# Performance work log

Measured on AMD Instinct MI355X. Metric: run time of the kernel, lower is better.

The kernel has to match this reference:

```python
import jax, jax.numpy as jnp
import numpy as np

T, B, D, H, OUT = 128, 256, 512, 768, 60


def setup_inputs() -> dict:
    key = jax.random.key(0)
    ks = jax.random.split(key, 8)
    def xavier(k, shape):
        fan_out, fan_in = shape
        limit = np.sqrt(6.0 / (fan_in + fan_out))
        return jax.random.uniform(k, shape, jnp.float32, -limit, limit)
    inp = {
        "input_sample": jax.random.normal(ks[0], (T, B, D), jnp.float32),
        # PyTorch LSTMCell params: weight_ih (4H, D), weight_hh (4H, H), biases (4H,)
        "W_ih": xavier(ks[1], (4 * H, D)),
        "W_hh": xavier(ks[2], (4 * H, H)),
        "b_ih": jax.random.uniform(ks[3], (4 * H,), jnp.float32, -1 / np.sqrt(H), 1 / np.sqrt(H)),
        "b_hh": jax.random.uniform(ks[4], (4 * H,), jnp.float32, -1 / np.sqrt(H), 1 / np.sqrt(H)),
        "W_fc": xavier(ks[5], (OUT, H)),
        "b_fc": jnp.zeros((OUT,), jnp.float32),
    }
    return inp


def _lstm_head(input_sample, W_ih, W_hh, b_ih, b_hh, W_fc, b_fc):
    B_ = input_sample.shape[1]
    H_ = W_hh.shape[1]
    # Precompute input projections for all time steps in one GEMM: (T, B, 4H)
    x_proj = jnp.einsum("tbd,gd->tbg", input_sample, W_ih) + b_ih + b_hh

    def step(carry, xp_t):
        h, c = carry
        gates = xp_t + h @ W_hh.T  # (B, 4H)
        i, f, g, o = jnp.split(gates, 4, axis=-1)  # PyTorch gate order: i, f, g, o
        i = jax.nn.sigmoid(i)
        f = jax.nn.sigmoid(f)
        g = jnp.tanh(g)
        o = jax.nn.sigmoid(o)
        c_new = f * c + i * g
        h_new = o * jnp.tanh(c_new)
        return (h_new, c_new), None

    h0 = jnp.zeros((B_, H_), input_sample.dtype)
    c0 = jnp.zeros((B_, H_), input_sample.dtype)
    (h_T, _), _ = jax.lax.scan(step, (h0, c0), x_proj)
    return h_T @ W_fc.T + b_fc  # (B, OUT)


def reference(input_sample, W_ih, W_hh, b_ih, b_hh, W_fc, b_fc):
    return _lstm_head(input_sample, W_ih, W_hh, b_ih, b_hh, W_fc, b_fc)
```

## Files before the change

### kernel.cpp

```cpp
#include <hip/hip_runtime.h>
#include <stdint.h>

#define T_ 128
#define B_ 256
#define D_ 512
#define H_ 768
#define OUT_ 60

using bf16x8 = __attribute__((ext_vector_type(8))) __bf16;
using f32x4  = __attribute__((ext_vector_type(4))) float;
using u32x4  = __attribute__((ext_vector_type(4))) unsigned int;

#define OFF_XPK  ((size_t)0)
#define OFF_WIPK (OFF_XPK + (size_t)T_*B_*D_*2)
#define OFF_WHPK (OFF_WIPK + (size_t)4*H_*D_*2)
#define OFF_H    (OFF_WHPK + (size_t)4*H_*H_*2)
#define OFF_HT   (OFF_H + (size_t)2*B_*H_*2)
#define OFF_BAR  (OFF_HT + (size_t)B_*H_*4)
#define OFF_END  (OFF_BAR + 65536)

__device__ __forceinline__ unsigned short f2bf(float f) {
  union { float f; unsigned u; } v; v.f = f;
  unsigned r = (v.u + 0x7fffu + ((v.u >> 16) & 1u)) >> 16;
  return (unsigned short)r;
}
__device__ __forceinline__ float sigf(float x) {
  return __builtin_amdgcn_rcpf(1.0f + __expf(-x));
}
__device__ __forceinline__ float tanhf_(float x) {
  return 2.0f * __builtin_amdgcn_rcpf(1.0f + __expf(-2.0f * x)) - 1.0f;
}
__device__ __forceinline__ void gload16(const void* g, void* l) {
  __builtin_amdgcn_global_load_lds(
      (const __attribute__((address_space(1))) unsigned int*)g,
      (__attribute__((address_space(3))) unsigned int*)l, 16, 0, 0);
}
template<int OFF, bool SC1>
__device__ __forceinline__ u32x4 ld16(const void* p) {
  u32x4 r;
  if constexpr (SC1)
    asm volatile("global_load_dwordx4 %0, %1, off offset:%c2 sc0 sc1"
                 : "=v"(r) : "v"(p), "i"(OFF) : "memory");
  else
    asm volatile("global_load_dwordx4 %0, %1, off offset:%c2 sc0"
                 : "=v"(r) : "v"(p), "i"(OFF) : "memory");
  return r;
}
template<bool SC1>
__device__ __forceinline__ unsigned ld4w(const unsigned* p) {
  unsigned r;
  if constexpr (SC1)
    asm volatile("global_load_dword %0, %1, off sc0 sc1\n\ts_waitcnt vmcnt(0)"
                 : "=v"(r) : "v"(p) : "memory");
  else
    asm volatile("global_load_dword %0, %1, off sc0\n\ts_waitcnt vmcnt(0)"
                 : "=v"(r) : "v"(p) : "memory");
  return r;
}
template<bool SC1>
__device__ __forceinline__ void st2(ushort* p, unsigned v) {
  if constexpr (SC1)
    asm volatile("global_store_short %0, %1, off sc0 sc1" :: "v"(p), "v"(v) : "memory");
  else
    asm volatile("global_store_short %0, %1, off sc0" :: "v"(p), "v"(v) : "memory");
}
template<bool SC1>
__device__ __forceinline__ void st4(unsigned* p, unsigned v) {
  if constexpr (SC1)
    asm volatile("global_store_dword %0, %1, off sc0 sc1" :: "v"(p), "v"(v) : "memory");
  else
    asm volatile("global_store_dword %0, %1, off sc0" :: "v"(p), "v"(v) : "memory");
}

__global__ void prep_kernel(const float* __restrict__ x,
                            const float* __restrict__ wihf,
                            const float* __restrict__ whhf,
                            uint8_t* __restrict__ ws) {
  ushort* xpk = (ushort*)(ws + OFF_XPK);
  ushort* wipk = (ushort*)(ws + OFF_WIPK);
  ushort* whpk = (ushort*)(ws + OFF_WHPK);
  unsigned* bar = (unsigned*)(ws + OFF_BAR);
  const size_t tid = (size_t)blockIdx.x * blockDim.x + threadIdx.x;
  const size_t nth = (size_t)gridDim.x * blockDim.x;

  for (size_t c = tid; c < (size_t)T_*B_*D_/8; c += nth) {
    const unsigned row = (unsigned)(c >> 6);
    const unsigned j = (unsigned)c & 63u;
    const unsigned t = row >> 8, b = row & 255u;
    const float4 v0 = ((const float4*)x)[c*2];
    const float4 v1 = ((const float4*)x)[c*2+1];
    ushort4 o0, o1;
    o0.x=f2bf(v0.x); o0.y=f2bf(v0.y); o0.z=f2bf(v0.z); o0.w=f2bf(v0.w);
    o1.x=f2bf(v1.x); o1.y=f2bf(v1.y); o1.z=f2bf(v1.z); o1.w=f2bf(v1.w);
    const size_t dst = ((size_t)(((t*8u + (b>>5))*2u + ((b>>4)&1u))*16u + (j>>2))*64u
                        + (j&3u)*16u + (b&15u)) * 8u;
    *(ushort4*)(xpk + dst)     = o0;
    *(ushort4*)(xpk + dst + 4) = o1;
  }
  for (size_t c = tid; c < (size_t)196608; c += nth) {
    const unsigned L = (unsigned)c & 63u;
    const unsigned r1 = (unsigned)(c >> 6);
    const unsigned nt = r1 % 6u, r2 = r1 / 6u;
    const unsigned kf = r2 & 15u, s = r2 >> 4;
    const unsigned i = nt*16u + (L & 15u);
    const unsigned G = (i & 3u)*768u + s*24u + (i >> 2);
    const unsigned k0 = kf*32u + (L >> 4)*8u;
    const float4 v0 = *(const float4*)(wihf + (size_t)G*512u + k0);
    const float4 v1 = *(const float4*)(wihf + (size_t)G*512u + k0 + 4);
    ushort4 o0, o1;
    o0.x=f2bf(v0.x); o0.y=f2bf(v0.y); o0.z=f2bf(v0.z); o0.w=f2bf(v0.w);
    o1.x=f2bf(v1.x); o1.y=f2bf(v1.y); o1.z=f2bf(v1.z); o1.w=f2bf(v1.w);
    *(ushort4*)(wipk + c*8)     = o0;
    *(ushort4*)(wipk + c*8 + 4) = o1;
  }
  for (size_t c = tid; c < (size_t)294912; c += nth) {
    const unsigned L = (unsigned)c & 63u;
    const unsigned r1 = (unsigned)(c >> 6);
    const unsigned nt = r1 % 6u, r2 = r1 / 6u;
    const unsigned kf = r2 % 24u, s = r2 / 24u;
    const unsigned i = nt*16u + (L & 15u);
    const unsigned G = (i & 3u)*768u + s*24u + (i >> 2);
    const unsigned k0 = kf*32u + (L >> 4)*8u;
    const float4 v0 = *(const float4*)(whhf + (size_t)G*768u + k0);
    const float4 v1 = *(const float4*)(whhf + (size_t)G*768u + k0 + 4);
    ushort4 o0, o1;
    o0.x=f2bf(v0.x); o0.y=f2bf(v0.y); o0.z=f2bf(v0.z); o0.w=f2bf(v0.w);
    o1.x=f2bf(v1.x); o1.y=f2bf(v1.y); o1.z=f2bf(v1.z); o1.w=f2bf(v1.w);
    *(ushort4*)(whpk + c*8)     = o0;
    *(ushort4*)(whpk + c*8 + 4) = o1;
  }
  for (size_t i = tid; i < 16384; i += nth) bar[i] = 0u;
}

template<bool SC1>
__device__ __forceinline__ void run_loop(uint8_t* ws, const ushort* whh_lds, float* gbuf,
                                         const float* bih, const float* bhh,
                                         int tid, int g, int s) {
  const int lane = tid & 63, w = tid >> 6, wq = w & 1, wm = w >> 1;
  const u32x4* xpkv = (const u32x4*)(ws + OFF_XPK);
  const u32x4* wipkv = (const u32x4*)(ws + OFF_WIPK);
  ushort* hb = (ushort*)(ws + OFF_H);
  float* hT = (float*)(ws + OFF_HT);
  unsigned* bar = (unsigned*)(ws + OFF_BAR);
  float* gw = gbuf + w*816;

  float bias[3][4];
  #pragma unroll
  for (int j = 0; j < 3; ++j) {
    const int col = s*24 + wq*12 + (lane >> 4) + 4*j;
    #pragma unroll
    for (int q = 0; q < 4; ++q) bias[j][q] = bih[q*H_ + col] + bhh[q*H_ + col];
  }
  const unsigned* fp = bar + (size_t)(g*32 + ((lane < 32) ? lane : 31)) * 16;

  f32x4 acc[3];
  float cc[3] = {0.f, 0.f, 0.f};

  auto xproj = [&](int tt) {
    #pragma unroll
    for (int n = 0; n < 3; ++n) acc[n] = (f32x4){0.f,0.f,0.f,0.f};
    const u32x4* xb2 = xpkv + ((((size_t)tt*8 + g)*2 + wm)*16)*64 + lane;
    const u32x4* wb2 = wipkv + ((size_t)(s*96 + wq*3))*64 + lane;
    #pragma unroll
    for (int kf = 0; kf < 16; ++kf) {
      const u32x4 xr = xb2[kf*64];
      const bf16x8 xa = *(const bf16x8*)&xr;
      #pragma unroll
      for (int n = 0; n < 3; ++n) {
        const u32x4 wr = wb2[(kf*6 + n)*64];
        acc[n] = __builtin_amdgcn_mfma_f32_16x16x32_bf16(xa, *(const bf16x8*)&wr, acc[n], 0, 0, 0);
      }
    }
  };

  xproj(0);
  #pragma unroll 1
  for (int t = 0; t < T_; ++t) {
    if (t > 0) {
      if (w == 0) {
        while (1) {
          const unsigned v = ld4w<SC1>(fp);
          if (__all((int)(v >= (unsigned)t))) break;
          __builtin_amdgcn_s_sleep(1);
        }
      }
      __syncthreads();
      const ushort* hr = hb + ((size_t)(t & 1)*8 + g)*((size_t)32*H_)
                         + (size_t)(wm*16 + (lane & 15))*H_ + (lane >> 4)*8;
      u32x4 ah[24];
      #define LH(i) ah[i] = ld16<(i)*64, SC1>(hr)
      LH(0); LH(1); LH(2); LH(3); LH(4); LH(5); LH(6); LH(7);
      LH(8); LH(9); LH(10); LH(11); LH(12); LH(13); LH(14); LH(15);
      LH(16); LH(17); LH(18); LH(19); LH(20); LH(21); LH(22); LH(23);
      #undef LH
      asm volatile("s_waitcnt vmcnt(0)" ::: "memory");
      __builtin_amdgcn_sched_barrier(0);
      #pragma unroll
      for (int kf = 0; kf < 24; ++kf) {
        const bf16x8 a = *(const bf16x8*)&ah[kf];
        #pragma unroll
        for (int n = 0; n < 3; ++n) {
          const bf16x8 b = *(const bf16x8*)(whh_lds + (size_t)((kf*6 + wq*3 + n)*64 + lane)*8);
          acc[n] = __builtin_amdgcn_mfma_f32_16x16x32_bf16(a, b, acc[n], 0, 0, 0);
        }
      }
    }
    #pragma unroll
    for (int n = 0; n < 3; ++n)
      #pragma unroll
      for (int r = 0; r < 4; ++r)
        gw[(n*16 + (lane & 15))*17 + (lane >> 4)*4 + r] = acc[n][r];
    float hv[3];
    #pragma unroll
    for (int j = 0; j < 3; ++j) {
      const int cl = (lane >> 4) + 4*j;
      const float g0 = gw[(cl*4+0)*17 + (lane & 15)];
      const float g1 = gw[(cl*4+1)*17 + (lane & 15)];
      const float g2 = gw[(cl*4+2)*17 + (lane & 15)];
      const float g3 = gw[(cl*4+3)*17 + (lane & 15)];
      const float iv = sigf(g0 + bias[j][0]);
      const float fv = sigf(g1 + bias[j][1]);
      const float gv = tanhf_(g2 + bias[j][2]);
      const float ov = sigf(g3 + bias[j][3]);
      const float cn = fv*cc[j] + iv*gv;
      cc[j] = cn;
      hv[j] = ov * tanhf_(cn);
    }
    const int rowl = wm*16 + (lane & 15);
    if (t == T_-1) {
      #pragma unroll
      for (int j = 0; j < 3; ++j) {
        const int col = s*24 + wq*12 + (lane >> 4) + 4*j;
        hT[(size_t)(g*32 + rowl)*H_ + col] = hv[j];
      }
      break;
    }
    ushort* hn = hb + ((size_t)((t+1) & 1)*8 + g)*((size_t)32*H_);
    #pragma unroll
    for (int j = 0; j < 3; ++j) {
      const int col = s*24 + wq*12 + (lane >> 4) + 4*j;
      st2<SC1>(hn + (size_t)rowl*H_ + col, (unsigned)f2bf(hv[j]));
    }
    asm volatile("s_waitcnt vmcnt(0)" ::: "memory");
    __syncthreads();
    if (tid == 0) st4<SC1>(bar + (size_t)(g*32 + s)*16, (unsigned)(t + 1));
    xproj(t + 1);
  }
}

__global__ __launch_bounds__(256, 1) void lstm_kernel(uint8_t* __restrict__ ws,
                                                      const float* __restrict__ bih,
                                                      const float* __restrict__ bhh) {
  __shared__ ushort whh_lds[73728];
  __shared__ float gbuf[3264];
  const int tid = threadIdx.x, lane = tid & 63, w = tid >> 6;
  const int g = blockIdx.x & 7, s = blockIdx.x >> 3;
  unsigned* bar = (unsigned*)(ws + OFF_BAR);

  const uint8_t* wsrc = ws + OFF_WHPK + (size_t)s*9216*16;
  #pragma unroll
  for (int i = 0; i < 36; ++i) {
    const int cb = (w*36 + i)*64;
    gload16(wsrc + (size_t)(cb + lane)*16, (uint8_t*)whh_lds + (size_t)cb*16);
  }

  const unsigned xcd = __builtin_amdgcn_s_getreg((3 << 11) | 20) & 7u;
  if (tid == 0) {
    unsigned one = 1u;
    asm volatile("global_store_dword %0, %1, off sc0" :: "v"(bar + 8192 + blockIdx.x*16), "v"(one) : "memory");
    asm volatile("global_store_dword %0, %1, off sc0 sc1" :: "v"(bar + 4096 + blockIdx.x), "v"(xcd) : "memory");
    asm volatile("s_waitcnt vmcnt(0)" ::: "memory");
    __hip_atomic_fetch_add(bar + 5120, 1u, __ATOMIC_RELAXED, __HIP_MEMORY_SCOPE_SYSTEM);
    while (__hip_atomic_load(bar + 5120, __ATOMIC_RELAXED, __HIP_MEMORY_SCOPE_SYSTEM) < 256u)
      __builtin_amdgcn_s_sleep(2);
  }
  __syncthreads();
  const int pl = (lane < 32) ? lane : 31;
  const unsigned oxcc = ld4w<true >(bar + 4096 + g + 8*pl);
  const unsigned otok = ld4w<false>(bar + 8192 + (size_t)(g + 8*pl)*16);
  const bool local = __all((int)(oxcc == xcd)) && __all((int)(otok == 1u));

  asm volatile("s_waitcnt vmcnt(0) lgkmcnt(0)" ::: "memory");
  __syncthreads();

  if (local) run_loop<false>(ws, whh_lds, gbuf, bih, bhh, tid, g, s);
  else       run_loop<true >(ws, whh_lds, gbuf, bih, bhh, tid, g, s);
}

__global__ __launch_bounds__(64) void fc_kernel(const uint8_t* __restrict__ ws,
                                                const float* __restrict__ wfc,
                                                const float* __restrict__ bfc,
                                                float* __restrict__ out) {
  const float* hT = (const float*)(ws + OFF_HT);
  const int b = blockIdx.x;
  const int lane = threadIdx.x;
  const float* hr = hT + (size_t)b*H_;
  float hv[12];
  #pragma unroll
  for (int i = 0; i < 12; ++i) hv[i] = hr[lane + i*64];
  for (int o = 0; o < OUT_; ++o) {
    const float* wr = wfc + (size_t)o*H_;
    float sum = 0.f;
    #pragma unroll
    for (int i = 0; i < 12; ++i) sum += hv[i] * wr[lane + i*64];
    #pragma unroll
    for (int off = 32; off; off >>= 1) sum += __shfl_xor(sum, off);
    if (lane == 0) out[(size_t)b*OUT_ + o] = sum + bfc[o];
  }
}

extern "C" void kernel_launch(void* const* d_in, const int* in_sizes, int n_in,
                              void* d_out, int out_size, void* d_ws, size_t ws_size,
                              hipStream_t stream) {
  const float* x   = (const float*)d_in[0];
  const float* wih = (const float*)d_in[1];
  const float* whh = (const float*)d_in[2];
  const float* bih = (const float*)d_in[3];
  const float* bhh = (const float*)d_in[4];
  const float* wfc = (const float*)d_in[5];
  const float* bfc = (const float*)d_in[6];
  uint8_t* ws = (uint8_t*)d_ws;
  float* out = (float*)d_out;

  prep_kernel<<<dim3(2048), dim3(256), 0, stream>>>(x, wih, whh, ws);
  lstm_kernel<<<dim3(256), dim3(256), 0, stream>>>(ws, bih, bhh);
  fc_kernel<<<dim3(256), dim3(64), 0, stream>>>(ws, wfc, bfc, out);
}
```

Measured before the change: 1.141 ms.

## Hoist input projection out of recurrent loop into a separate bf16 GEMM kernel

Moves the per-timestep input projection (x·W_ih) out of the serial LSTM recurrence into a standalone tiled MFMA GEMM kernel that writes bf16 gate pre-activations for all timesteps. The recurrent loop then only loads 12 precomputed values per lane per step, which shortens the serial critical path between barrier waits. This costs an extra kernel launch, a large bf16 intermediate buffer written to and read back from global memory, and bf16 rounding of the projection. The change also simplifies the locality check and makes the flag load/store always use sc1 coherence.

After: 994.0 us. 12.9% less time.

```diff
diff --git a/kernel.cpp b/kernel.cpp
--- a/kernel.cpp
+++ b/kernel.cpp
@@ -5,19 +5,21 @@
 #define B_ 256
 #define D_ 512
 #define H_ 768
+#define NG 3072
 #define OUT_ 60
 
 using bf16x8 = __attribute__((ext_vector_type(8))) __bf16;
 using f32x4  = __attribute__((ext_vector_type(4))) float;
 using u32x4  = __attribute__((ext_vector_type(4))) unsigned int;
 
-#define OFF_XPK  ((size_t)0)
-#define OFF_WIPK (OFF_XPK + (size_t)T_*B_*D_*2)
-#define OFF_WHPK (OFF_WIPK + (size_t)4*H_*D_*2)
-#define OFF_H    (OFF_WHPK + (size_t)4*H_*H_*2)
+#define OFF_XB   ((size_t)0)
+#define OFF_WI   (OFF_XB + (size_t)T_*B_*D_*2)
+#define OFF_WHPK (OFF_WI + (size_t)NG*D_*2)
+#define OFF_H    (OFF_WHPK + (size_t)NG*H_*2)
 #define OFF_HT   (OFF_H + (size_t)2*B_*H_*2)
 #define OFF_BAR  (OFF_HT + (size_t)B_*H_*4)
-#define OFF_END  (OFF_BAR + 65536)
+#define OFF_XP   (OFF_BAR + 65536)
+#define OFF_END  (OFF_XP + (size_t)T_*B_*NG*2)
 
 __device__ __forceinline__ unsigned short f2bf(float f) {
   union { float f; unsigned u; } v; v.f = f;
@@ -46,15 +48,10 @@
                  : "=v"(r) : "v"(p), "i"(OFF) : "memory");
   return r;
 }
-template<bool SC1>
-__device__ __forceinline__ unsigned ld4w(const unsigned* p) {
+__device__ __forceinline__ unsigned ld4coh(const unsigned* p) {
   unsigned r;
-  if constexpr (SC1)
-    asm volatile("global_load_dword %0, %1, off sc0 sc1\n\ts_waitcnt vmcnt(0)"
-                 : "=v"(r) : "v"(p) : "memory");
-  else
-    asm volatile("global_load_dword %0, %1, off sc0\n\ts_waitcnt vmcnt(0)"
-                 : "=v"(r) : "v"(p) : "memory");
+  asm volatile("global_load_dword %0, %1, off sc0 sc1\n\ts_waitcnt vmcnt(0)"
+               : "=v"(r) : "v"(p) : "memory");
   return r;
 }
 template<bool SC1>
@@ -64,54 +61,30 @@
   else
     asm volatile("global_store_short %0, %1, off sc0" :: "v"(p), "v"(v) : "memory");
 }
-template<bool SC1>
-__device__ __forceinline__ void st4(unsigned* p, unsigned v) {
-  if constexpr (SC1)
-    asm volatile("global_store_dword %0, %1, off sc0 sc1" :: "v"(p), "v"(v) : "memory");
-  else
-    asm volatile("global_store_dword %0, %1, off sc0" :: "v"(p), "v"(v) : "memory");
+__device__ __forceinline__ void st4coh(unsigned* p, unsigned v) {
+  asm volatile("global_store_dword %0, %1, off sc0 sc1" :: "v"(p), "v"(v) : "memory");
 }
 
 __global__ void prep_kernel(const float* __restrict__ x,
                             const float* __restrict__ wihf,
                             const float* __restrict__ whhf,
                             uint8_t* __restrict__ ws) {
-  ushort* xpk = (ushort*)(ws + OFF_XPK);
-  ushort* wipk = (ushort*)(ws + OFF_WIPK);
+  ushort* xb = (ushort*)(ws + OFF_XB);
+  ushort* wi = (ushort*)(ws + OFF_WI);
   ushort* whpk = (ushort*)(ws + OFF_WHPK);
   unsigned* bar = (unsigned*)(ws + OFF_BAR);
   const size_t tid = (size_t)blockIdx.x * blockDim.x + threadIdx.x;
   const size_t nth = (size_t)gridDim.x * blockDim.x;
 
-  for (size_t c = tid; c < (size_t)T_*B_*D_/8; c += nth) {
-    const unsigned row = (unsigned)(c >> 6);
-    const unsigned j = (unsigned)c & 63u;
-    const unsigned t = row >> 8, b = row & 255u;
-    const float4 v0 = ((const float4*)x)[c*2];
-    const float4 v1 = ((const float4*)x)[c*2+1];
-    ushort4 o0, o1;
-    o0.x=f2bf(v0.x); o0.y=f2bf(v0.y); o0.z=f2bf(v0.z); o0.w=f2bf(v0.w);
-    o1.x=f2bf(v1.x); o1.y=f2bf(v1.y); o1.z=f2bf(v1.z); o1.w=f2bf(v1.w);
-    const size_t dst = ((size_t)(((t*8u + (b>>5))*2u + ((b>>4)&1u))*16u + (j>>2))*64u
-                        + (j&3u)*16u + (b&15u)) * 8u;
-    *(ushort4*)(xpk + dst)     = o0;
-    *(ushort4*)(xpk + dst + 4) = o1;
-  }
-  for (size_t c = tid; c < (size_t)196608; c += nth) {
-    const unsigned L = (unsigned)c & 63u;
-    const unsigned r1 = (unsigned)(c >> 6);
-    const unsigned nt = r1 % 6u, r2 = r1 / 6u;
-    const unsigned kf = r2 & 15u, s = r2 >> 4;
-    const unsigned i = nt*16u + (L & 15u);
-    const unsigned G = (i & 3u)*768u + s*24u + (i >> 2);
-    const unsigned k0 = kf*32u + (L >> 4)*8u;
-    const float4 v0 = *(const float4*)(wihf + (size_t)G*512u + k0);
-    const float4 v1 = *(const float4*)(wihf + (size_t)G*512u + k0 + 4);
-    ushort4 o0, o1;
-    o0.x=f2bf(v0.x); o0.y=f2bf(v0.y); o0.z=f2bf(v0.z); o0.w=f2bf(v0.w);
-    o1.x=f2bf(v1.x); o1.y=f2bf(v1.y); o1.z=f2bf(v1.z); o1.w=f2bf(v1.w);
-    *(ushort4*)(wipk + c*8)     = o0;
-    *(ushort4*)(wipk + c*8 + 4) = o1;
+  for (size_t i = tid; i < (size_t)T_*B_*D_/4; i += nth) {
+    float4 v = ((const float4*)x)[i];
+    ushort4 o; o.x=f2bf(v.x); o.y=f2bf(v.y); o.z=f2bf(v.z); o.w=f2bf(v.w);
+    ((ushort4*)xb)[i] = o;
+  }
+  for (size_t i = tid; i < (size_t)NG*D_/4; i += nth) {
+    float4 v = ((const float4*)wihf)[i];
+    ushort4 o; o.x=f2bf(v.x); o.y=f2bf(v.y); o.z=f2bf(v.z); o.w=f2bf(v.w);
+    ((ushort4*)wi)[i] = o;
   }
   for (size_t c = tid; c < (size_t)294912; c += nth) {
     const unsigned L = (unsigned)c & 63u;
@@ -132,14 +105,80 @@
   for (size_t i = tid; i < 16384; i += nth) bar[i] = 0u;
 }
 
+__global__ __launch_bounds__(256) void xproj_kernel(uint8_t* __restrict__ ws) {
+  const ushort* __restrict__ xb = (const ushort*)(ws + OFF_XB);
+  const ushort* __restrict__ wi = (const ushort*)(ws + OFF_WI);
+  ushort* __restrict__ xp = (ushort*)(ws + OFF_XP);
+
+  __shared__ ushort smA[128*64];
+  __shared__ ushort smB[128*64];
+
+  const int tid = threadIdx.x;
+  const int lane = tid & 63;
+  const int w = tid >> 6;
+  const int bn = blockIdx.x % 24;
+  const int bm = blockIdx.x / 24;
+  const int m0 = bm * 128, n0 = bn * 128;
+  const int mi = (w >> 1) * 64, ni = (w & 1) * 64;
+
+  f32x4 acc[4][4] = {};
+
+  for (int k0 = 0; k0 < D_; k0 += 64) {
+    __syncthreads();
+    #pragma unroll
+    for (int i = 0; i < 4; ++i) {
+      const int ig = w*4 + i;
+      const int o  = ig*1024 + lane*16;
+      const int row = o >> 7;
+      const int colB = o & 127;
+      const int scol = colB ^ ((row & 7) << 4);
+      gload16((const uint8_t*)xb + ((size_t)(m0+row)*D_ + k0)*2 + scol,
+              (uint8_t*)smA + ig*1024);
+      gload16((const uint8_t*)wi + ((size_t)(n0+row)*D_ + k0)*2 + scol,
+              (uint8_t*)smB + ig*1024);
+    }
+    __syncthreads();
+    #pragma unroll
+    for (int kk = 0; kk < 2; ++kk) {
+      const int colB = kk*64 + (lane >> 4)*16;
+      bf16x8 a[4], b[4];
+      #pragma unroll
+      for (int mt = 0; mt < 4; ++mt) {
+        const int row = mi + mt*16 + (lane & 15);
+        a[mt] = *(const bf16x8*)((const uint8_t*)smA + row*128 + (colB ^ ((row & 7) << 4)));
+      }
+      #pragma unroll
+      for (int nt = 0; nt < 4; ++nt) {
+        const int row = ni + nt*16 + (lane & 15);
+        b[nt] = *(const bf16x8*)((const uint8_t*)smB + row*128 + (colB ^ ((row & 7) << 4)));
+      }
+      #pragma unroll
+      for (int mt = 0; mt < 4; ++mt)
+        #pragma unroll
+        for (int nt = 0; nt < 4; ++nt)
+          acc[mt][nt] = __builtin_amdgcn_mfma_f32_16x16x32_bf16(a[mt], b[nt], acc[mt][nt], 0, 0, 0);
+    }
+  }
+  #pragma unroll
+  for (int mt = 0; mt < 4; ++mt)
+    #pragma unroll
+    for (int nt = 0; nt < 4; ++nt) {
+      const int r0 = m0 + mi + mt*16 + (lane >> 4)*4;
+      const int c  = n0 + ni + nt*16 + (lane & 15);
+      #pragma unroll
+      for (int r = 0; r < 4; ++r)
+        xp[(size_t)(r0 + r)*NG + c] = f2bf(acc[mt][nt][r]);
+    }
+}
+
 template<bool SC1>
 __device__ __forceinline__ void run_loop(uint8_t* ws, const ushort* whh_lds, float* gbuf,
                                          const float* bih, const float* bhh,
                                          int tid, int g, int s) {
   const int lane = tid & 63, w = tid >> 6, wq = w & 1, wm = w >> 1;
-  const u32x4* xpkv = (const u32x4*)(ws + OFF_XPK);
-  const u32x4* wipkv = (const u32x4*)(ws + OFF_WIPK);
+  const int l15 = lane & 15, hi = lane >> 4;
   ushort* hb = (ushort*)(ws + OFF_H);
+  const ushort* xp = (const ushort*)(ws + OFF_XP);
   float* hT = (float*)(ws + OFF_HT);
   unsigned* bar = (unsigned*)(ws + OFF_BAR);
   float* gw = gbuf + w*816;
@@ -147,46 +186,39 @@
   float bias[3][4];
   #pragma unroll
   for (int j = 0; j < 3; ++j) {
-    const int col = s*24 + wq*12 + (lane >> 4) + 4*j;
+    const int col = s*24 + wq*12 + hi + 4*j;
     #pragma unroll
     for (int q = 0; q < 4; ++q) bias[j][q] = bih[q*H_ + col] + bhh[q*H_ + col];
   }
   const unsigned* fp = bar + (size_t)(g*32 + ((lane < 32) ? lane : 31)) * 16;
 
-  f32x4 acc[3];
+  const ushort* xpb = xp + (size_t)(g*32 + wm*16 + l15)*NG + s*24 + wq*12 + hi;
+  ushort xq[12];
+  {
+    const ushort* p = xpb;
+    #pragma unroll
+    for (int q = 0; q < 4; ++q)
+      #pragma unroll
+      for (int j = 0; j < 3; ++j)
+        xq[q*3+j] = p[q*768 + 4*j];
+  }
+
   float cc[3] = {0.f, 0.f, 0.f};
 
-  auto xproj = [&](int tt) {
-    #pragma unroll
-    for (int n = 0; n < 3; ++n) acc[n] = (f32x4){0.f,0.f,0.f,0.f};
-    const u32x4* xb2 = xpkv + ((((size_t)tt*8 + g)*2 + wm)*16)*64 + lane;
-    const u32x4* wb2 = wipkv + ((size_t)(s*96 + wq*3))*64 + lane;
-    #pragma unroll
-    for (int kf = 0; kf < 16; ++kf) {
-      const u32x4 xr = xb2[kf*64];
-      const bf16x8 xa = *(const bf16x8*)&xr;
-      #pragma unroll
-      for (int n = 0; n < 3; ++n) {
-        const u32x4 wr = wb2[(kf*6 + n)*64];
-        acc[n] = __builtin_amdgcn_mfma_f32_16x16x32_bf16(xa, *(const bf16x8*)&wr, acc[n], 0, 0, 0);
-      }
-    }
-  };
-
-  xproj(0);
   #pragma unroll 1
   for (int t = 0; t < T_; ++t) {
+    f32x4 acc[3] = {};
     if (t > 0) {
       if (w == 0) {
         while (1) {
-          const unsigned v = ld4w<SC1>(fp);
+          const unsigned v = ld4coh(fp);
           if (__all((int)(v >= (unsigned)t))) break;
           __builtin_amdgcn_s_sleep(1);
         }
       }
       __syncthreads();
       const ushort* hr = hb + ((size_t)(t & 1)*8 + g)*((size_t)32*H_)
-                         + (size_t)(wm*16 + (lane & 15))*H_ + (lane >> 4)*8;
+                         + (size_t)(wm*16 + l15)*H_ + hi*8;
       u32x4 ah[24];
       #define LH(i) ah[i] = ld16<(i)*64, SC1>(hr)
       LH(0); LH(1); LH(2); LH(3); LH(4); LH(5); LH(6); LH(7);
@@ -209,28 +241,30 @@
     for (int n = 0; n < 3; ++n)
       #pragma unroll
       for (int r = 0; r < 4; ++r)
-        gw[(n*16 + (lane & 15))*17 + (lane >> 4)*4 + r] = acc[n][r];
+        gw[(n*16 + l15)*17 + hi*4 + r] = acc[n][r];
     float hv[3];
     #pragma unroll
     for (int j = 0; j < 3; ++j) {
-      const int cl = (lane >> 4) + 4*j;
-      const float g0 = gw[(cl*4+0)*17 + (lane & 15)];
-      const float g1 = gw[(cl*4+1)*17 + (lane & 15)];
-      const float g2 = gw[(cl*4+2)*17 + (lane & 15)];
-      const float g3 = gw[(cl*4+3)*17 + (lane & 15)];
-      const float iv = sigf(g0 + bias[j][0]);
-      const float fv = sigf(g1 + bias[j][1]);
-      const float gv = tanhf_(g2 + bias[j][2]);
-      const float ov = sigf(g3 + bias[j][3]);
+      const int cl = hi + 4*j;
+      float gq[4];
+      #pragma unroll
+      for (int q = 0; q < 4; ++q) {
+        union { unsigned u; float f; } xv; xv.u = ((unsigned)xq[q*3 + j]) << 16;
+        gq[q] = gw[(cl*4+q)*17 + l15] + xv.f + bias[j][q];
+      }
+      const float iv = sigf(gq[0]);
+      const float fv = sigf(gq[1]);
+      const float gv = tanhf_(gq[2]);
+      const float ov = sigf(gq[3]);
       const float cn = fv*cc[j] + iv*gv;
       cc[j] = cn;
       hv[j] = ov * tanhf_(cn);
     }
-    const int rowl = wm*16 + (lane & 15);
+    const int rowl = wm*16 + l15;
     if (t == T_-1) {
       #pragma unroll
       for (int j = 0; j < 3; ++j) {
-        const int col = s*24 + wq*12 + (lane >> 4) + 4*j;
+        const int col = s*24 + wq*12 + hi + 4*j;
         hT[(size_t)(g*32 + rowl)*H_ + col] = hv[j];
       }
       break;
@@ -238,13 +272,20 @@
     ushort* hn = hb + ((size_t)((t+1) & 1)*8 + g)*((size_t)32*H_);
     #pragma unroll
     for (int j = 0; j < 3; ++j) {
-      const int col = s*24 + wq*12 + (lane >> 4) + 4*j;
+      const int col = s*24 + wq*12 + hi + 4*j;
       st2<SC1>(hn + (size_t)rowl*H_ + col, (unsigned)f2bf(hv[j]));
     }
     asm volatile("s_waitcnt vmcnt(0)" ::: "memory");
     __syncthreads();
-    if (tid == 0) st4<SC1>(bar + (size_t)(g*32 + s)*16, (unsigned)(t + 1));
-    xproj(t + 1);
+    if (tid == 0) st4coh(bar + (size_t)(g*32 + s)*16, (unsigned)(t + 1));
+    {
+      const ushort* p = xpb + (size_t)(t + 1)*B_*NG;
+      #pragma unroll
+      for (int q = 0; q < 4; ++q)
+        #pragma unroll
+        for (int j = 0; j < 3; ++j)
+          xq[q*3+j] = p[q*768 + 4*j];
+    }
   }
 }
 
@@ -266,9 +307,7 @@
 
   const unsigned xcd = __builtin_amdgcn_s_getreg((3 << 11) | 20) & 7u;
   if (tid == 0) {
-    unsigned one = 1u;
-    asm volatile("global_store_dword %0, %1, off sc0" :: "v"(bar + 8192 + blockIdx.x*16), "v"(one) : "memory");
-    asm volatile("global_store_dword %0, %1, off sc0 sc1" :: "v"(bar + 4096 + blockIdx.x), "v"(xcd) : "memory");
+    st4coh(bar + 4096 + blockIdx.x, xcd);
     asm volatile("s_waitcnt vmcnt(0)" ::: "memory");
     __hip_atomic_fetch_add(bar + 5120, 1u, __ATOMIC_RELAXED, __HIP_MEMORY_SCOPE_SYSTEM);
     while (__hip_atomic_load(bar + 5120, __ATOMIC_RELAXED, __HIP_MEMORY_SCOPE_SYSTEM) < 256u)
@@ -276,9 +315,8 @@
   }
   __syncthreads();
   const int pl = (lane < 32) ? lane : 31;
-  const unsigned oxcc = ld4w<true >(bar + 4096 + g + 8*pl);
-  const unsigned otok = ld4w<false>(bar + 8192 + (size_t)(g + 8*pl)*16);
-  const bool local = __all((int)(oxcc == xcd)) && __all((int)(otok == 1u));
+  const unsigned oxcc = ld4coh(bar + 4096 + g + 8*pl);
+  const bool local = __all((int)(oxcc == xcd));
 
   asm volatile("s_waitcnt vmcnt(0) lgkmcnt(0)" ::: "memory");
   __syncthreads();
@@ -323,6 +361,7 @@
   float* out = (float*)d_out;
 
   prep_kernel<<<dim3(2048), dim3(256), 0, stream>>>(x, wih, whh, ws);
+  xproj_kernel<<<dim3(256*24), dim3(256), 0, stream>>>(ws);
   lstm_kernel<<<dim3(256), dim3(256), 0, stream>>>(ws, bih, bhh);
   fc_kernel<<<dim3(256), dim3(64), 0, stream>>>(ws, wfc, bfc, out);
 }
```
